# Kernel tuning notes

Hardware: AMD Instinct MI355X
Metric: run time of the kernel (lower is better)

The kernel has to match this reference:

```python
import jax, jax.numpy as jnp
import numpy as np

B, T, H, UNITS = 32, 2048, 1024, 1024
NEG_BIG = -1e9

def setup_inputs() -> dict:
    key = jax.random.key(0)
    k1, k2, k3, k4 = jax.random.split(key, 4)
    enc_hs = jax.random.normal(k1, (B, T, H), dtype=jnp.float32)
    dec_ht = jax.random.normal(k2, (B, H), dtype=jnp.float32)
    mask = jax.random.randint(k3, (B, T), 0, 2).astype(jnp.bool_)
    # Dense(units, use_bias=False) kernel: (H, UNITS), he_normal-like scale
    Wa = jax.random.normal(k4, (H, UNITS), dtype=jnp.float32) * np.sqrt(2.0 / H)
    return {"enc_hs": enc_hs, "dec_ht": dec_ht, "mask": mask, "Wa": Wa}

def reference(enc_hs, dec_ht, mask, Wa):
    # mask-apply on encoder states: (B,T,H) * (B,T,1)
    enc = enc_hs * mask[:, :, None].astype(enc_hs.dtype)
    # 'general' score: dec_ht @ (enc @ Wa)^T  -> (B,T)
    proj = jnp.einsum('bth,hu->btu', enc, Wa)           # (B,T,UNITS)
    score = jnp.einsum('bh,bth->bt', dec_ht, proj)      # (B,T)
    # additive mask: where mask is False, add -1e9
    score = score + (~mask).astype(score.dtype) * NEG_BIG
    attn = jax.nn.softmax(score, axis=-1)               # (B,T)
    # context = attn-weighted sum of masked encoder states -> (B,H)
    context = jnp.einsum('bt,bth->bh', attn, enc)
    return context
```

## Files before the change

kernel.cpp:

```cpp
#include <hip/hip_runtime.h>
#include <math.h>
#include <cstdint>
#include <cstddef>

#define BB 32
#define TT 2048
#define HH 1024
#define UU 1024
#define NBK 32
#define BT 64
#define WT 16
#define NEG_BIG (-1e9f)

__global__ __launch_bounds__(256) void k_v(const float* __restrict__ Wa,
                                           const float* __restrict__ dec,
                                           float* __restrict__ v) {
    __shared__ float lds[4 * UU];
    const int tid = threadIdx.x;
    const int h0  = blockIdx.x * 4;

    const float4* Wa4  = reinterpret_cast<const float4*>(Wa + (size_t)h0 * UU);
    float4*       lds4 = reinterpret_cast<float4*>(lds);
    #pragma unroll
    for (int i = 0; i < 4; ++i)
        lds4[i * 256 + tid] = Wa4[i * 256 + tid];
    __syncthreads();

    const int wid = tid >> 6, lane = tid & 63;
    for (int j = 0; j < 8; ++j) {
        const int b = wid * 8 + j;
        const float4* d4 = reinterpret_cast<const float4*>(dec + (size_t)b * UU);
        float4 dreg[4];
        #pragma unroll
        for (int k = 0; k < 4; ++k) dreg[k] = d4[k * 64 + lane];

        float p[4];
        #pragma unroll
        for (int r = 0; r < 4; ++r) {
            float acc = 0.f;
            #pragma unroll
            for (int k = 0; k < 4; ++k) {
                const float4 a = lds4[r * 256 + k * 64 + lane];
                acc += a.x * dreg[k].x + a.y * dreg[k].y +
                       a.z * dreg[k].z + a.w * dreg[k].w;
            }
            p[r] = acc;
        }
        #pragma unroll
        for (int r = 0; r < 4; ++r) {
            #pragma unroll
            for (int off = 32; off > 0; off >>= 1)
                p[r] += __shfl_xor(p[r], off, 64);
        }
        if (lane == 0) {
            #pragma unroll
            for (int r = 0; r < 4; ++r)
                v[(size_t)b * HH + h0 + r] = p[r];
        }
    }
}

__global__ __launch_bounds__(256, 4) void k_flash(const float* __restrict__ enc,
                                                  const int* __restrict__ mask,
                                                  const float* __restrict__ v,
                                                  float* __restrict__ pm,
                                                  float* __restrict__ pl,
                                                  float* __restrict__ pctx) {
    const int tid  = threadIdx.x;
    const int wid  = tid >> 6, lane = tid & 63;
    const int bk   = blockIdx.x;
    const int b    = bk >> 5;
    const int c    = bk & (NBK - 1);
    const int t0   = c * BT + wid * WT;

    const float4* v4 = reinterpret_cast<const float4*>(v + (size_t)b * HH);
    float4 vr[4];
    #pragma unroll
    for (int k = 0; k < 4; ++k) vr[k] = v4[k * 64 + lane];

    const int* mrow = mask + (size_t)b * TT + t0;
    int mv[WT];
    #pragma unroll
    for (int t = 0; t < WT; ++t) mv[t] = mrow[t];

    float m = -INFINITY, l = 0.f;
    float4 ctx[4];
    #pragma unroll
    for (int k = 0; k < 4; ++k) ctx[k] = make_float4(0.f, 0.f, 0.f, 0.f);

    const float4* erow = reinterpret_cast<const float4*>(
                             enc + ((size_t)b * TT + t0) * HH);

    #pragma unroll 4
    for (int t = 0; t < WT; ++t) {
        if (mv[t]) {
            float4 e[4];
            #pragma unroll
            for (int k = 0; k < 4; ++k)
                e[k] = erow[(size_t)t * 256 + k * 64 + lane];

            float p = 0.f;
            #pragma unroll
            for (int k = 0; k < 4; ++k)
                p += e[k].x * vr[k].x + e[k].y * vr[k].y +
                     e[k].z * vr[k].z + e[k].w * vr[k].w;
            #pragma unroll
            for (int off = 32; off > 0; off >>= 1)
                p += __shfl_xor(p, off, 64);

            const float mnew  = fmaxf(m, p);
            const float alpha = __expf(m - mnew);
            const float pe    = __expf(p - mnew);
            l = l * alpha + pe;
            #pragma unroll
            for (int k = 0; k < 4; ++k) {
                ctx[k].x = ctx[k].x * alpha + pe * e[k].x;
                ctx[k].y = ctx[k].y * alpha + pe * e[k].y;
                ctx[k].z = ctx[k].z * alpha + pe * e[k].z;
                ctx[k].w = ctx[k].w * alpha + pe * e[k].w;
            }
            m = mnew;
        } else {
            const float mnew  = fmaxf(m, NEG_BIG);
            const float alpha = __expf(m - mnew);
            l = l * alpha + __expf(NEG_BIG - mnew);
            m = mnew;
        }
    }

    __shared__ float4 sctx[4 * 256];
    __shared__ float  sm[4], sl[4];
    #pragma unroll
    for (int k = 0; k < 4; ++k)
        sctx[wid * 256 + k * 64 + lane] = ctx[k];
    if (lane == 0) { sm[wid] = m; sl[wid] = l; }
    __syncthreads();

    const float M  = fmaxf(fmaxf(sm[0], sm[1]), fmaxf(sm[2], sm[3]));
    const float a0 = __expf(sm[0] - M), a1 = __expf(sm[1] - M);
    const float a2 = __expf(sm[2] - M), a3 = __expf(sm[3] - M);
    const float L  = sl[0] * a0 + sl[1] * a1 + sl[2] * a2 + sl[3] * a3;

    const float4 x0 = sctx[tid], x1 = sctx[256 + tid];
    const float4 x2 = sctx[512 + tid], x3 = sctx[768 + tid];
    float4 r;
    r.x = a0 * x0.x + a1 * x1.x + a2 * x2.x + a3 * x3.x;
    r.y = a0 * x0.y + a1 * x1.y + a2 * x2.y + a3 * x3.y;
    r.z = a0 * x0.z + a1 * x1.z + a2 * x2.z + a3 * x3.z;
    r.w = a0 * x0.w + a1 * x1.w + a2 * x2.w + a3 * x3.w;

    reinterpret_cast<float4*>(pctx + (size_t)bk * HH)[tid] = r;
    if (tid == 0) { pm[bk] = M; pl[bk] = L; }
}

__global__ __launch_bounds__(256) void k_reduce(const float* __restrict__ pm,
                                                const float* __restrict__ pl,
                                                const float* __restrict__ pctx,
                                                float* __restrict__ out) {
    const int b = blockIdx.x;
    const int h = blockIdx.y * 256 + threadIdx.x;
    __shared__ float sm[NBK], sl[NBK];

    if (threadIdx.x < NBK) {
        sm[threadIdx.x] = pm[b * NBK + threadIdx.x];
        sl[threadIdx.x] = pl[b * NBK + threadIdx.x];
    }
    __syncthreads();

    float M = -INFINITY;
    #pragma unroll
    for (int c = 0; c < NBK; ++c) M = fmaxf(M, sm[c]);

    float L = 0.f, acc = 0.f;
    #pragma unroll 4
    for (int c = 0; c < NBK; ++c) {
        const float e = __expf(sm[c] - M);
        L   += sl[c] * e;
        acc += e * pctx[((size_t)b * NBK + c) * HH + h];
    }

    out[(size_t)b * HH + h] = acc / L;
}

extern "C" void kernel_launch(void* const* d_in, const int* in_sizes, int n_in,
                              void* d_out, int out_size, void* d_ws, size_t ws_size,
                              hipStream_t stream) {
    const float* enc  = (const float*)d_in[0];
    const float* dec  = (const float*)d_in[1];
    const int*   mask = (const int*)  d_in[2];
    const float* Wa   = (const float*)d_in[3];
    float*       out  = (float*)d_out;

    float* ws   = (float*)d_ws;
    float* v    = ws;
    float* pm   = v  + (size_t)BB * HH;
    float* pl   = pm + (size_t)BB * NBK;
    float* pctx = pl + (size_t)BB * NBK;

    k_v<<<HH / 4, 256, 0, stream>>>(Wa, dec, v);
    k_flash<<<BB * NBK, 256, 0, stream>>>(enc, mask, v, pm, pl, pctx);
    dim3 g2(BB, HH / 256);
    k_reduce<<<g2, 256, 0, stream>>>(pm, pl, pctx, out);
}
```

Measured before the change: 347.3 us.

## Fuse final reduction into flash kernel, skip masked rows via ballot, halve k_v rows

Makes k_v compute two rows of v per block instead of four, launching twice as many blocks. In k_flash, the per-row mask loop becomes a ballot bitmask, and only unmasked rows are iterated, with an all-masked fallback that sets m=-1e9 and l=count. The separate reduce kernel is removed: an atomic per-batch counter lets the last block of each batch merge the partials, at the cost of a memset launch and a threadfence handshake. Intent is to cut launch overhead and drop divergent handling of masked rows.

```diff
diff --git a/kernel.cpp b/kernel.cpp
--- a/kernel.cpp
+++ b/kernel.cpp
@@ -15,14 +15,14 @@
 __global__ __launch_bounds__(256) void k_v(const float* __restrict__ Wa,
                                            const float* __restrict__ dec,
                                            float* __restrict__ v) {
-    __shared__ float lds[4 * UU];
+    __shared__ float lds[2 * UU];
     const int tid = threadIdx.x;
-    const int h0  = blockIdx.x * 4;
+    const int h0  = blockIdx.x * 2;
 
     const float4* Wa4  = reinterpret_cast<const float4*>(Wa + (size_t)h0 * UU);
     float4*       lds4 = reinterpret_cast<float4*>(lds);
     #pragma unroll
-    for (int i = 0; i < 4; ++i)
+    for (int i = 0; i < 2; ++i)
         lds4[i * 256 + tid] = Wa4[i * 256 + tid];
     __syncthreads();
 
@@ -34,9 +34,9 @@
         #pragma unroll
         for (int k = 0; k < 4; ++k) dreg[k] = d4[k * 64 + lane];
 
-        float p[4];
-        #pragma unroll
-        for (int r = 0; r < 4; ++r) {
+        float p[2];
+        #pragma unroll
+        for (int r = 0; r < 2; ++r) {
             float acc = 0.f;
             #pragma unroll
             for (int k = 0; k < 4; ++k) {
@@ -47,15 +47,14 @@
             p[r] = acc;
         }
         #pragma unroll
-        for (int r = 0; r < 4; ++r) {
+        for (int r = 0; r < 2; ++r) {
             #pragma unroll
             for (int off = 32; off > 0; off >>= 1)
                 p[r] += __shfl_xor(p[r], off, 64);
         }
         if (lane == 0) {
-            #pragma unroll
-            for (int r = 0; r < 4; ++r)
-                v[(size_t)b * HH + h0 + r] = p[r];
+            v[(size_t)b * HH + h0]     = p[0];
+            v[(size_t)b * HH + h0 + 1] = p[1];
         }
     }
 }
@@ -65,7 +64,9 @@
                                                   const float* __restrict__ v,
                                                   float* __restrict__ pm,
                                                   float* __restrict__ pl,
-                                                  float* __restrict__ pctx) {
+                                                  float* __restrict__ pctx,
+                                                  int* __restrict__ cnt,
+                                                  float* __restrict__ out) {
     const int tid  = threadIdx.x;
     const int wid  = tid >> 6, lane = tid & 63;
     const int bk   = blockIdx.x;
@@ -79,9 +80,9 @@
     for (int k = 0; k < 4; ++k) vr[k] = v4[k * 64 + lane];
 
     const int* mrow = mask + (size_t)b * TT + t0;
-    int mv[WT];
-    #pragma unroll
-    for (int t = 0; t < WT; ++t) mv[t] = mrow[t];
+    const int  myb  = (lane < WT) ? mrow[lane] : 0;
+    unsigned   bits = (unsigned)(__ballot(myb != 0) & 0xFFFFu);
+    const int  nmask = WT - __popc(bits);
 
     float m = -INFINITY, l = 0.f;
     float4 ctx[4];
@@ -91,45 +92,45 @@
     const float4* erow = reinterpret_cast<const float4*>(
                              enc + ((size_t)b * TT + t0) * HH);
 
-    #pragma unroll 4
-    for (int t = 0; t < WT; ++t) {
-        if (mv[t]) {
-            float4 e[4];
-            #pragma unroll
-            for (int k = 0; k < 4; ++k)
-                e[k] = erow[(size_t)t * 256 + k * 64 + lane];
-
-            float p = 0.f;
-            #pragma unroll
-            for (int k = 0; k < 4; ++k)
-                p += e[k].x * vr[k].x + e[k].y * vr[k].y +
-                     e[k].z * vr[k].z + e[k].w * vr[k].w;
-            #pragma unroll
-            for (int off = 32; off > 0; off >>= 1)
-                p += __shfl_xor(p, off, 64);
-
-            const float mnew  = fmaxf(m, p);
-            const float alpha = __expf(m - mnew);
-            const float pe    = __expf(p - mnew);
-            l = l * alpha + pe;
-            #pragma unroll
-            for (int k = 0; k < 4; ++k) {
-                ctx[k].x = ctx[k].x * alpha + pe * e[k].x;
-                ctx[k].y = ctx[k].y * alpha + pe * e[k].y;
-                ctx[k].z = ctx[k].z * alpha + pe * e[k].z;
-                ctx[k].w = ctx[k].w * alpha + pe * e[k].w;
-            }
-            m = mnew;
-        } else {
-            const float mnew  = fmaxf(m, NEG_BIG);
-            const float alpha = __expf(m - mnew);
-            l = l * alpha + __expf(NEG_BIG - mnew);
-            m = mnew;
-        }
+    while (bits) {
+        const int t = __ffs(bits) - 1;
+        bits &= bits - 1;
+
+        float4 e[4];
+        #pragma unroll
+        for (int k = 0; k < 4; ++k)
+            e[k] = erow[(size_t)t * 256 + k * 64 + lane];
+
+        float p = 0.f;
+        #pragma unroll
+        for (int k = 0; k < 4; ++k)
+            p += e[k].x * vr[k].x + e[k].y * vr[k].y +
+                 e[k].z * vr[k].z + e[k].w * vr[k].w;
+        #pragma unroll
+        for (int off = 32; off > 0; off >>= 1)
+            p += __shfl_xor(p, off, 64);
+
+        const float mnew  = fmaxf(m, p);
+        const float alpha = __expf(m - mnew);
+        const float pe    = __expf(p - mnew);
+        l = l * alpha + pe;
+        #pragma unroll
+        for (int k = 0; k < 4; ++k) {
+            ctx[k].x = ctx[k].x * alpha + pe * e[k].x;
+            ctx[k].y = ctx[k].y * alpha + pe * e[k].y;
+            ctx[k].z = ctx[k].z * alpha + pe * e[k].z;
+            ctx[k].w = ctx[k].w * alpha + pe * e[k].w;
+        }
+        m = mnew;
+    }
+    if (m == -INFINITY) {
+        m = NEG_BIG;
+        l = (float)nmask;
     }
 
     __shared__ float4 sctx[4 * 256];
     __shared__ float  sm[4], sl[4];
+    __shared__ int    sLast;
     #pragma unroll
     for (int k = 0; k < 4; ++k)
         sctx[wid * 256 + k * 64 + lane] = ctx[k];
@@ -151,35 +152,42 @@
 
     reinterpret_cast<float4*>(pctx + (size_t)bk * HH)[tid] = r;
     if (tid == 0) { pm[bk] = M; pl[bk] = L; }
-}
-
-__global__ __launch_bounds__(256) void k_reduce(const float* __restrict__ pm,
-                                                const float* __restrict__ pl,
-                                                const float* __restrict__ pctx,
-                                                float* __restrict__ out) {
-    const int b = blockIdx.x;
-    const int h = blockIdx.y * 256 + threadIdx.x;
-    __shared__ float sm[NBK], sl[NBK];
-
-    if (threadIdx.x < NBK) {
-        sm[threadIdx.x] = pm[b * NBK + threadIdx.x];
-        sl[threadIdx.x] = pl[b * NBK + threadIdx.x];
-    }
-    __syncthreads();
-
-    float M = -INFINITY;
-    #pragma unroll
-    for (int c = 0; c < NBK; ++c) M = fmaxf(M, sm[c]);
-
-    float L = 0.f, acc = 0.f;
+
+    __syncthreads();
+    if (tid == 0) {
+        __threadfence();
+        sLast = (atomicAdd(&cnt[b], 1) == NBK - 1);
+    }
+    __syncthreads();
+    if (!sLast) return;
+    __threadfence();
+
+    __shared__ float fm[NBK], fl[NBK];
+    if (tid < NBK) {
+        fm[tid] = pm[b * NBK + tid];
+        fl[tid] = pl[b * NBK + tid];
+    }
+    __syncthreads();
+
+    float FM = -INFINITY;
+    #pragma unroll
+    for (int k = 0; k < NBK; ++k) FM = fmaxf(FM, fm[k]);
+
+    const float4* p4 = reinterpret_cast<const float4*>(pctx) +
+                       (size_t)b * NBK * 256 + tid;
+    float FL = 0.f;
+    float4 acc = make_float4(0.f, 0.f, 0.f, 0.f);
     #pragma unroll 4
-    for (int c = 0; c < NBK; ++c) {
-        const float e = __expf(sm[c] - M);
-        L   += sl[c] * e;
-        acc += e * pctx[((size_t)b * NBK + c) * HH + h];
-    }
-
-    out[(size_t)b * HH + h] = acc / L;
+    for (int k = 0; k < NBK; ++k) {
+        const float e = __expf(fm[k] - FM);
+        FL += fl[k] * e;
+        const float4 x = p4[k * 256];
+        acc.x += e * x.x; acc.y += e * x.y;
+        acc.z += e * x.z; acc.w += e * x.w;
+    }
+    const float inv = 1.f / FL;
+    acc.x *= inv; acc.y *= inv; acc.z *= inv; acc.w *= inv;
+    reinterpret_cast<float4*>(out)[(size_t)b * 256 + tid] = acc;
 }
 
 extern "C" void kernel_launch(void* const* d_in, const int* in_sizes, int n_in,
@@ -195,10 +203,10 @@
     float* v    = ws;
     float* pm   = v  + (size_t)BB * HH;
     float* pl   = pm + (size_t)BB * NBK;
-    float* pctx = pl + (size_t)BB * NBK;
-
-    k_v<<<HH / 4, 256, 0, stream>>>(Wa, dec, v);
-    k_flash<<<BB * NBK, 256, 0, stream>>>(enc, mask, v, pm, pl, pctx);
-    dim3 g2(BB, HH / 256);
-    k_reduce<<<g2, 256, 0, stream>>>(pm, pl, pctx, out);
+    int*   cnt  = (int*)(pl + (size_t)BB * NBK);
+    float* pctx = pl + (size_t)BB * NBK + 1024;
+
+    hipMemsetAsync(cnt, 0, BB * sizeof(int), stream);
+    k_v<<<HH / 2, 256, 0, stream>>>(Wa, dec, v);
+    k_flash<<<BB * NBK, 256, 0, stream>>>(enc, mask, v, pm, pl, pctx, cnt, out);
 }
```

Measured after the change: 399.8 us. 15.1% more time.
